# Optimization experiments

Measured on AMD Instinct MI355X. Metric: run time of the kernel, lower is better.

Reference implementation:

```python
import jax, jax.numpy as jnp
import numpy as np

BATCH, IN_DIM, OUT_DIM, DEGREE = 4096, 1024, 1024, 7


def setup_inputs() -> dict:
    key = jax.random.key(0)
    k1, k2 = jax.random.split(key)
    std = 1.0 / (IN_DIM * (DEGREE + 1))
    return {
        "x": jax.random.normal(k1, (BATCH, IN_DIM), dtype=jnp.float32),
        "a": jnp.zeros((1,), dtype=jnp.float32),
        "q": jnp.ones((1,), dtype=jnp.float32),
        "coeffs": jax.random.normal(k2, (IN_DIM, OUT_DIM, DEGREE + 1), dtype=jnp.float32) * std,
    }


def reference(x, a, q, coeffs):
    # x: [B, I]; a, q: [1]; coeffs: [I, O, D+1]
    xt = jnp.tanh(x)
    n_basis = coeffs.shape[-1]  # degree + 1
    # Iterative three-term recurrence (avoids the exponential naive recursion):
    # P0 = 1; P1 = x - a; Pn = (x - (a + q^n)) P_{n-1} - a q^{n-1} P_{n-2}
    basis = [jnp.ones_like(xt)]
    if n_basis > 1:
        basis.append(xt - a)
    for n in range(2, n_basis):
        pn = (xt - (a + q ** n)) * basis[-1] - a * (q ** (n - 1)) * basis[-2]
        basis.append(pn)
    B = jnp.stack(basis, axis=-1)  # [B, I, D+1]
    y = jnp.einsum('bid,iod->bo', B, coeffs)
    return y
```

## Files before the change

### kernel.cpp

```cpp
#include <hip/hip_runtime.h>

#define BATCH   4096
#define IN_DIM  1024
#define OUT_DIM 1024
#define NB      8
#define NBK     7
#define KD2     (IN_DIM * NBK)

typedef __bf16 bf16x8 __attribute__((ext_vector_type(8)));
typedef float  f32x4  __attribute__((ext_vector_type(4)));
typedef unsigned short us8 __attribute__((ext_vector_type(8)));
typedef unsigned short us4 __attribute__((ext_vector_type(4)));

__device__ __forceinline__ unsigned short f2bf(float f) {
    unsigned int u = __float_as_uint(f);
    u += 0x7fffu + ((u >> 16) & 1u);
    return (unsigned short)(u >> 16);
}

__device__ __forceinline__ float fast_tanh(float x) {
    const float LOG2E_X2 = 2.8853900817779268f;
    float e = __builtin_amdgcn_exp2f(x * LOG2E_X2);
    return 1.0f - 2.0f * __builtin_amdgcn_rcpf(e + 1.0f);
}

__device__ __forceinline__ void ld_lds16(const unsigned short* g, unsigned short* l) {
    __builtin_amdgcn_global_load_lds(
        (const __attribute__((address_space(1))) void*)g,
        (__attribute__((address_space(3))) void*)l, 16, 0, 0);
}

#define BASIS_BLOCKS (BATCH / 2)

__global__ __launch_bounds__(256) void basis_kernel(
    const float* __restrict__ x, const float* __restrict__ ap,
    const float* __restrict__ qp, unsigned short* __restrict__ Aw) {
    const int tid = threadIdx.x;
    const float a = ap[0], q = qp[0];
    const int b  = blockIdx.x * 2 + (tid >> 7);
    const int i0 = (tid & 127) * 8;

    const float* xs = x + (size_t)b * IN_DIM + i0;
    float4 v0 = *(const float4*)xs;
    float4 v1 = *(const float4*)(xs + 4);

    float xe[8] = {v0.x, v0.y, v0.z, v0.w, v1.x, v1.y, v1.z, v1.w};
    float pm2[8], pm1[8];
    us8 ov;
#pragma unroll
    for (int e = 0; e < 8; ++e) {
        xe[e] = fast_tanh(xe[e]);
        pm2[e] = 1.0f;
        pm1[e] = xe[e] - a;
        ov[e] = f2bf(pm1[e]);
    }
    unsigned short* arow = Aw + (size_t)b * KD2 + i0;
    *(us8*)arow = ov;
    float qn = q, qn1 = 1.0f;
#pragma unroll
    for (int n = 2; n < NB; ++n) {
        qn *= q; qn1 *= q;
#pragma unroll
        for (int e = 0; e < 8; ++e) {
            float pn = (xe[e] - (a + qn)) * pm1[e] - a * qn1 * pm2[e];
            pm2[e] = pm1[e]; pm1[e] = pn;
            ov[e] = f2bf(pn);
        }
        *(us8*)(arow + (size_t)(n - 1) * IN_DIM) = ov;
    }
}

#define REPACK_BLOCKS 512
#define TI 32
#define TO 64
#define RSTR 232

__global__ __launch_bounds__(256) void repack_kernel(
    const float* __restrict__ coeffs,
    unsigned short* __restrict__ Bt,
    float* __restrict__ bias_part) {
    __shared__ __align__(16) unsigned short lt[TO * RSTR + 512];
    const int tid = threadIdx.x;
    const int bid = blockIdx.x;
    const int g  = bid & 31;
    const int i0 = g * TI;
    const int o0 = (bid >> 5) * TO;
    const int o_local = tid & 63;
    float bpart = 0.f;
#pragma unroll
    for (int pass = 0; pass < 8; ++pass) {
        const int i_local = pass * 4 + (tid >> 6);
        const float* src = coeffs +
            ((size_t)(i0 + i_local) * OUT_DIM + (o0 + o_local)) * NB;
        float4 v0 = *(const float4*)src;
        float4 v1 = *(const float4*)(src + 4);
        bpart += v0.x;
        unsigned short* dst = lt + o_local * RSTR + i_local;
        dst[0]   = f2bf(v0.y); dst[32]  = f2bf(v0.z); dst[64]  = f2bf(v0.w);
        dst[96]  = f2bf(v1.x); dst[128] = f2bf(v1.y); dst[160] = f2bf(v1.z);
        dst[192] = f2bf(v1.w);
    }
    float* sb = (float*)(lt + TO * RSTR);
    sb[(tid >> 6) * 64 + o_local] = bpart;
    __syncthreads();
    if (tid < 64)
        bias_part[(size_t)g * OUT_DIM + o0 + tid] =
            sb[tid] + sb[64 + tid] + sb[128 + tid] + sb[192 + tid];
#pragma unroll
    for (int p = 0; p < 7; ++p) {
        const int o = tid >> 2;
        const int c = tid & 3;
        us8 v = *(const us8*)(lt + o * RSTR + p * 32 + c * 8);
        *(us8*)(Bt + (size_t)(o0 + o) * KD2 + (size_t)p * IN_DIM + i0 + c * 8) = v;
    }
}

#define ZERO_BLOCKS   (BATCH * OUT_DIM / 4096)

__global__ __launch_bounds__(256) void zero_kernel(float* __restrict__ C) {
    float* dst = C + (size_t)blockIdx.x * 4096 + threadIdx.x * 4;
    const f32x4 zero = {0.f, 0.f, 0.f, 0.f};
#pragma unroll
    for (int j = 0; j < 4; ++j) *(f32x4*)(dst + j * 1024) = zero;
}

#define BM 128
#define BN 128
#define BK 64
#define KSPLIT 4
#define KCH (KD2 / KSPLIT)

#define GEMM_BODY(EPILOGUE)                                                    \
    __shared__ __align__(16) unsigned short lA[BM * BK];            \
    __shared__ __align__(16) unsigned short lB[BN * BK];            \
    const int tid  = threadIdx.x;                                              \
    const int bidx = blockIdx.x;                                               \
    const int m0 = (((bidx >> 3) & 3) * 8 + (bidx & 7)) * BM;                  \
    const int n0 = ((bidx >> 5) & 7) * BN;                                     \
    const int ch = bidx >> 8;                                                  \
    const size_t kb = (size_t)ch * KCH;                                        \
    const int lane  = tid & 63;                                                \
    const int wid   = tid >> 6;                                                \
    const int wm    = (wid & 1) * 64;                                          \
    const int wn    = (wid >> 1) * 64;                                         \
    const int row16 = lane & 15;                                               \
    const int quad  = lane >> 4;                                               \
    int aOff[4], bOff[4];                                                      \
    _Pragma("unroll") for (int mt = 0; mt < 4; ++mt) {                         \
        int r = wm + mt * 16 + row16;                                          \
        aOff[mt] = r * BK + ((quad ^ (r & 7)) * 8);                            \
    }                                                                          \
    _Pragma("unroll") for (int nt = 0; nt < 4; ++nt) {                         \
        int c = wn + nt * 16 + row16;                                          \
        bOff[nt] = c * BK + ((quad ^ (c & 7)) * 8);                            \
    }                                                                          \
    const int r0 = tid >> 3, s0 = tid & 7;                                     \
    const unsigned short* gA0 = A  + (size_t)(m0 + r0) * KD2 + kb              \
                                + ((s0 ^ (r0 & 7)) * 8);                       \
    const unsigned short* gB0 = Bt + (size_t)(n0 + r0) * KD2 + kb              \
                                + ((s0 ^ (r0 & 7)) * 8);                       \
    unsigned short* dA = lA + tid * 8;                                         \
    unsigned short* dB = lB + tid * 8;                                         \
    f32x4 acc[4][4] = {};                                                      \
    for (int k0 = 0; k0 < KCH; k0 += BK) {                                     \
        _Pragma("unroll") for (int j = 0; j < 4; ++j)                          \
            ld_lds16(gA0 + k0 + (size_t)j * 32 * KD2, dA + j * 2048);          \
        _Pragma("unroll") for (int j = 0; j < 4; ++j)                          \
            ld_lds16(gB0 + k0 + (size_t)j * 32 * KD2, dB + j * 2048);          \
        __syncthreads();                                                       \
        _Pragma("unroll") for (int kk = 0; kk < 2; ++kk) {                     \
            const int xo = kk * 32;                                            \
            bf16x8 aF[4], bF[4];                                               \
            _Pragma("unroll") for (int mt = 0; mt < 4; ++mt)                   \
                aF[mt] = *(const bf16x8*)(lA + (aOff[mt] ^ xo));               \
            _Pragma("unroll") for (int nt = 0; nt < 4; ++nt)                   \
                bF[nt] = *(const bf16x8*)(lB + (bOff[nt] ^ xo));               \
            _Pragma("unroll") for (int mt = 0; mt < 4; ++mt)                   \
                _Pragma("unroll") for (int nt = 0; nt < 4; ++nt)               \
                    acc[mt][nt] = __builtin_amdgcn_mfma_f32_16x16x32_bf16(     \
                        aF[mt], bF[nt], acc[mt][nt], 0, 0, 0);                 \
        }                                                                      \
        __syncthreads();                                                       \
    }                                                                          \
    if (ch == 0) {                                                             \
        float* sbw = (float*)lA;      \
        if (tid < BN) {                                                        \
            float s = 0.f;                                                     \
            _Pragma("unroll") for (int g = 0; g < 32; ++g)                     \
                s += bias_part[(size_t)g * OUT_DIM + n0 + tid];                \
            sbw[tid] = s;                                                      \
        }                                                                      \
        __syncthreads();                                                       \
    }                                                                          \
    const float* sb = (const float*)lA;                                        \
    EPILOGUE

__global__ __launch_bounds__(256, 4) void gemm_store(
    const unsigned short* __restrict__ A,
    const unsigned short* __restrict__ Bt,
    const float* __restrict__ bias_part,
    float* __restrict__ Cp,
    float* __restrict__ C) {
    GEMM_BODY(
        float* dst = (ch == 0) ? C : (Cp + (size_t)(ch - 1) * BATCH * OUT_DIM);
        _Pragma("unroll") for (int mt = 0; mt < 4; ++mt) {
            const int rbase = m0 + wm + mt * 16 + quad * 4;
            _Pragma("unroll") for (int nt = 0; nt < 4; ++nt) {
                const int col = n0 + wn + nt * 16 + row16;
                const float bv = (ch == 0) ? sb[wn + nt * 16 + row16] : 0.f;
                _Pragma("unroll") for (int r = 0; r < 4; ++r)
                    dst[(size_t)(rbase + r) * OUT_DIM + col] =
                        acc[mt][nt][r] + bv;
            }
        }
    )
}

__global__ __launch_bounds__(256, 4) void gemm_atomic(
    const unsigned short* __restrict__ A,
    const unsigned short* __restrict__ Bt,
    const float* __restrict__ bias_part,
    float* __restrict__ C) {
    GEMM_BODY(
        _Pragma("unroll") for (int mt = 0; mt < 4; ++mt) {
            const int rbase = m0 + wm + mt * 16 + quad * 4;
            _Pragma("unroll") for (int nt = 0; nt < 4; ++nt) {
                const int col = n0 + wn + nt * 16 + row16;
                const float bv = (ch == 0) ? sb[wn + nt * 16 + row16] : 0.f;
                _Pragma("unroll") for (int r = 0; r < 4; ++r)
                    atomicAdd(&C[(size_t)(rbase + r) * OUT_DIM + col],
                              acc[mt][nt][r] + bv);
            }
        }
    )
}

__global__ __launch_bounds__(256) void reduce_kernel(
    const float* __restrict__ Cp,
    float* __restrict__ C) {
    const size_t P = (size_t)BATCH * OUT_DIM;
    const size_t base = (size_t)blockIdx.x * 4096 + threadIdx.x * 4;
#pragma unroll
    for (int j = 0; j < 4; ++j) {
        const size_t idx = base + (size_t)j * 1024;
        f32x4 v  = *(const f32x4*)(C + idx);
        f32x4 v1 = *(const f32x4*)(Cp + idx);
        f32x4 v2 = *(const f32x4*)(Cp + P + idx);
        f32x4 v3 = *(const f32x4*)(Cp + 2 * P + idx);
        v = v + v1 + v2 + v3;
        *(f32x4*)(C + idx) = v;
    }
}

__global__ __launch_bounds__(256) void fallback_kernel(
    const float* __restrict__ x, const float* __restrict__ ap,
    const float* __restrict__ qp, const float* __restrict__ coeffs,
    float* __restrict__ out) {
    __shared__ float sb[IN_DIM][NB];
    const int b = blockIdx.x;
    const float a = ap[0], q = qp[0];
    for (int i = threadIdx.x; i < IN_DIM; i += 256) {
        float xt = fast_tanh(x[(size_t)b * IN_DIM + i]);
        float p0 = 1.0f, p1 = xt - a;
        sb[i][0] = p0; sb[i][1] = p1;
        float qn = q, qn1 = 1.0f;
#pragma unroll
        for (int n = 2; n < NB; ++n) {
            qn *= q; qn1 *= q;
            float p2 = (xt - (a + qn)) * p1 - a * qn1 * p0;
            sb[i][n] = p2;
            p0 = p1; p1 = p2;
        }
    }
    __syncthreads();
    float acc[4] = {0.f, 0.f, 0.f, 0.f};
    for (int i = 0; i < IN_DIM; ++i) {
        float bb[NB];
#pragma unroll
        for (int d = 0; d < NB; ++d) bb[d] = sb[i][d];
#pragma unroll
        for (int j = 0; j < 4; ++j) {
            int o = threadIdx.x + j * 256;
            const float* cf = coeffs + ((size_t)i * OUT_DIM + o) * NB;
            float s = 0.f;
#pragma unroll
            for (int d = 0; d < NB; ++d) s += bb[d] * cf[d];
            acc[j] += s;
        }
    }
#pragma unroll
    for (int j = 0; j < 4; ++j)
        out[(size_t)b * OUT_DIM + threadIdx.x + j * 256] = acc[j];
}

extern "C" void kernel_launch(void* const* d_in, const int* in_sizes, int n_in,
                              void* d_out, int out_size, void* d_ws, size_t ws_size,
                              hipStream_t stream) {
    const float* x      = (const float*)d_in[0];
    const float* a      = (const float*)d_in[1];
    const float* q      = (const float*)d_in[2];
    const float* coeffs = (const float*)d_in[3];
    float* out = (float*)d_out;

    const size_t needA = (size_t)BATCH * KD2 * sizeof(unsigned short);
    const size_t needB = (size_t)OUT_DIM * KD2 * sizeof(unsigned short);
    const size_t needBias = 32 * (size_t)OUT_DIM * sizeof(float);
    const size_t needCp = 3 * (size_t)BATCH * OUT_DIM * sizeof(float);

    if (ws_size >= needA + needB + needBias + needCp) {
        unsigned short* Aw = (unsigned short*)d_ws;
        unsigned short* Bt = Aw + (size_t)BATCH * KD2;
        float* bias_part = (float*)((char*)d_ws + needA + needB);
        float* Cp = (float*)((char*)d_ws + needA + needB + needBias);
        basis_kernel<<<BASIS_BLOCKS, 256, 0, stream>>>(x, a, q, Aw);
        repack_kernel<<<REPACK_BLOCKS, 256, 0, stream>>>(coeffs, Bt, bias_part);
        gemm_store<<<(BATCH / BM) * (OUT_DIM / BN) * KSPLIT, 256, 0, stream>>>(
            Aw, Bt, bias_part, Cp, out);
        reduce_kernel<<<BATCH * OUT_DIM / 4096, 256, 0, stream>>>(Cp, out);
    } else if (ws_size >= needA + needB + needBias) {
        unsigned short* Aw = (unsigned short*)d_ws;
        unsigned short* Bt = Aw + (size_t)BATCH * KD2;
        float* bias_part = (float*)((char*)d_ws + needA + needB);
        basis_kernel<<<BASIS_BLOCKS, 256, 0, stream>>>(x, a, q, Aw);
        repack_kernel<<<REPACK_BLOCKS, 256, 0, stream>>>(coeffs, Bt, bias_part);
        zero_kernel<<<ZERO_BLOCKS, 256, 0, stream>>>(out);
        gemm_atomic<<<(BATCH / BM) * (OUT_DIM / BN) * KSPLIT, 256, 0, stream>>>(
            Aw, Bt, bias_part, out);
    } else {
        fallback_kernel<<<BATCH, 256, 0, stream>>>(x, a, q, coeffs, out);
    }
}
```

Baseline: 180.2 us.

## Fuse split-K reduction into GEMM via last-arriving-block counters

Drops the separate reduce kernel. Each GEMM block bumps a per-tile atomic counter after writing its partial, and the fourth block to arrive for a tile sums the three partial buffers into the output. The counters are zeroed by the basis kernel. This saves a kernel launch and lets the reduction overlap with GEMM tail work. In exchange it adds fences, an atomic and an extra barrier to every block, and the final reduction is done by only one block per tile.

```diff
diff --git a/kernel.cpp b/kernel.cpp
--- a/kernel.cpp
+++ b/kernel.cpp
@@ -34,8 +34,10 @@
 
 __global__ __launch_bounds__(256) void basis_kernel(
     const float* __restrict__ x, const float* __restrict__ ap,
-    const float* __restrict__ qp, unsigned short* __restrict__ Aw) {
+    const float* __restrict__ qp, unsigned short* __restrict__ Aw,
+    unsigned int* flags) {
     const int tid = threadIdx.x;
+    if (flags && blockIdx.x == 0) flags[tid] = 0u;
     const float a = ap[0], q = qp[0];
     const int b  = blockIdx.x * 2 + (tid >> 7);
     const int i0 = (tid & 127) * 8;
@@ -130,7 +132,7 @@
 #define KSPLIT 4
 #define KCH (KD2 / KSPLIT)
 
-#define GEMM_BODY(EPILOGUE)                                                    \
+#define GEMM_BODY(...)                                                         \
     __shared__ __align__(16) unsigned short lA[BM * BK];            \
     __shared__ __align__(16) unsigned short lB[BN * BK];            \
     const int tid  = threadIdx.x;                                              \
@@ -193,13 +195,14 @@
         __syncthreads();                                                       \
     }                                                                          \
     const float* sb = (const float*)lA;                                        \
-    EPILOGUE
+    __VA_ARGS__
 
 __global__ __launch_bounds__(256, 4) void gemm_store(
     const unsigned short* __restrict__ A,
     const unsigned short* __restrict__ Bt,
     const float* __restrict__ bias_part,
     float* __restrict__ Cp,
+    unsigned int* flags,
     float* __restrict__ C) {
     GEMM_BODY(
         float* dst = (ch == 0) ? C : (Cp + (size_t)(ch - 1) * BATCH * OUT_DIM);
@@ -211,6 +214,28 @@
                 _Pragma("unroll") for (int r = 0; r < 4; ++r)
                     dst[(size_t)(rbase + r) * OUT_DIM + col] =
                         acc[mt][nt][r] + bv;
+            }
+        }
+        __threadfence();
+        __syncthreads();
+        __shared__ int s_last;
+        if (tid == 0)
+            s_last = (atomicAdd(&flags[bidx & 255], 1u) == 3u) ? 1 : 0;
+        __syncthreads();
+        if (s_last) {
+            __threadfence();
+            const size_t P = (size_t)BATCH * OUT_DIM;
+            const int rr = tid >> 5;
+            const int cc = (tid & 31) * 4;
+            _Pragma("unroll 1") for (int p = 0; p < 16; ++p) {
+                const size_t idx =
+                    (size_t)(m0 + p * 8 + rr) * OUT_DIM + n0 + cc;
+                f32x4 v  = *(volatile const f32x4*)(C + idx);
+                f32x4 v1 = *(volatile const f32x4*)(Cp + idx);
+                f32x4 v2 = *(volatile const f32x4*)(Cp + P + idx);
+                f32x4 v3 = *(volatile const f32x4*)(Cp + 2 * P + idx);
+                f32x4 s = v + v1 + v2 + v3;
+                *(f32x4*)(C + idx) = s;
             }
         }
     )
@@ -235,23 +260,6 @@
     )
 }
 
-__global__ __launch_bounds__(256) void reduce_kernel(
-    const float* __restrict__ Cp,
-    float* __restrict__ C) {
-    const size_t P = (size_t)BATCH * OUT_DIM;
-    const size_t base = (size_t)blockIdx.x * 4096 + threadIdx.x * 4;
-#pragma unroll
-    for (int j = 0; j < 4; ++j) {
-        const size_t idx = base + (size_t)j * 1024;
-        f32x4 v  = *(const f32x4*)(C + idx);
-        f32x4 v1 = *(const f32x4*)(Cp + idx);
-        f32x4 v2 = *(const f32x4*)(Cp + P + idx);
-        f32x4 v3 = *(const f32x4*)(Cp + 2 * P + idx);
-        v = v + v1 + v2 + v3;
-        *(f32x4*)(C + idx) = v;
-    }
-}
-
 __global__ __launch_bounds__(256) void fallback_kernel(
     const float* __restrict__ x, const float* __restrict__ ap,
     const float* __restrict__ qp, const float* __restrict__ coeffs,
@@ -305,23 +313,24 @@
     const size_t needA = (size_t)BATCH * KD2 * sizeof(unsigned short);
     const size_t needB = (size_t)OUT_DIM * KD2 * sizeof(unsigned short);
     const size_t needBias = 32 * (size_t)OUT_DIM * sizeof(float);
+    const size_t needFlags = 256 * sizeof(unsigned int);
     const size_t needCp = 3 * (size_t)BATCH * OUT_DIM * sizeof(float);
 
-    if (ws_size >= needA + needB + needBias + needCp) {
+    if (ws_size >= needA + needB + needBias + needFlags + needCp) {
         unsigned short* Aw = (unsigned short*)d_ws;
         unsigned short* Bt = Aw + (size_t)BATCH * KD2;
         float* bias_part = (float*)((char*)d_ws + needA + needB);
-        float* Cp = (float*)((char*)d_ws + needA + needB + needBias);
-        basis_kernel<<<BASIS_BLOCKS, 256, 0, stream>>>(x, a, q, Aw);
+        unsigned int* flags = (unsigned int*)((char*)d_ws + needA + needB + needBias);
+        float* Cp = (float*)((char*)d_ws + needA + needB + needBias + needFlags);
+        basis_kernel<<<BASIS_BLOCKS, 256, 0, stream>>>(x, a, q, Aw, flags);
         repack_kernel<<<REPACK_BLOCKS, 256, 0, stream>>>(coeffs, Bt, bias_part);
         gemm_store<<<(BATCH / BM) * (OUT_DIM / BN) * KSPLIT, 256, 0, stream>>>(
-            Aw, Bt, bias_part, Cp, out);
-        reduce_kernel<<<BATCH * OUT_DIM / 4096, 256, 0, stream>>>(Cp, out);
+            Aw, Bt, bias_part, Cp, flags, out);
     } else if (ws_size >= needA + needB + needBias) {
         unsigned short* Aw = (unsigned short*)d_ws;
         unsigned short* Bt = Aw + (size_t)BATCH * KD2;
         float* bias_part = (float*)((char*)d_ws + needA + needB);
-        basis_kernel<<<BASIS_BLOCKS, 256, 0, stream>>>(x, a, q, Aw);
+        basis_kernel<<<BASIS_BLOCKS, 256, 0, stream>>>(x, a, q, Aw, nullptr);
         repack_kernel<<<REPACK_BLOCKS, 256, 0, stream>>>(coeffs, Bt, bias_part);
         zero_kernel<<<ZERO_BLOCKS, 256, 0, stream>>>(out);
         gemm_atomic<<<(BATCH / BM) * (OUT_DIM / BN) * KSPLIT, 256, 0, stream>>>(
```

Measured after the change: 375.0 us. 108% more time.
